# Kernel optimization log

Measured on AMD Instinct MI355X. Metric: run time of the kernel, lower is better.

Reference implementation:

```python
import jax, jax.numpy as jnp
import numpy as np

N = 100000
E = 50000
NNZ = 300000
F_IN = 128
F_OUT = 128


def setup_inputs() -> dict:
    key = jax.random.key(0)
    ks = jax.random.split(key, 10)
    X = jax.random.normal(ks[0], (N, F_IN), dtype=jnp.float32)
    X0 = jax.random.normal(ks[1], (N, F_IN), dtype=jnp.float32)
    vertex = jax.random.randint(ks[2], (NNZ,), 0, N, dtype=jnp.int32)
    edges = jax.random.randint(ks[3], (NNZ,), 0, E, dtype=jnp.int32)
    # params init per reset_parameters: uniform(0.02, 0.05)
    u = lambda k, s: jax.random.uniform(k, s, jnp.float32, 0.02, 0.05)
    w_b = u(ks[4], (2 * F_IN, F_OUT))
    w_a = u(ks[5], (2 * F_IN, F_OUT))
    w_c = u(ks[6], (2 * F_IN, F_OUT))
    b_b = u(ks[7], (1, F_OUT))
    b_a = u(ks[8], (1, F_OUT))
    b_c = u(ks[9], (1, F_OUT))
    return {"X": X, "vertex": vertex, "edges": edges, "X0": X0,
            "n_edges": E, "w_b": w_b, "w_a": w_a, "w_c": w_c,
            "b_b": b_b, "b_a": b_a, "b_c": b_c}


def reference(X, vertex, edges, X0, n_edges, w_b, w_a, w_c, b_b, b_a, b_c):
    n = X.shape[-2]
    # round 1: node -> hyperedge aggregation (scatter-add by edge id)
    Xve = X[vertex]                                        # [nnz, F]
    Xe = jax.ops.segment_sum(Xve, edges, num_segments=n_edges)  # [E, F]
    # round 2: hyperedge -> node, concat with gathered node features
    Xev = jnp.concatenate([X[vertex], Xe[edges]], axis=-1)  # [nnz, 2F]
    Xv = jax.ops.segment_sum(Xev, vertex, num_segments=n)   # [N, 2F]
    # normalization is Identity (InputNorm=False)
    center = Xv @ w_b + b_b                 # [N, F_OUT]
    aXv = jnp.abs(Xv)
    scope_l = aXv @ w_a + b_a
    scope_r = aXv @ w_c + b_c
    HL = center - scope_l
    HR = center + scope_r
    return (center, HL, HR)
```

## Files before the change

kernel.cpp:

```cpp
#include <hip/hip_runtime.h>
#include <cstddef>
#include <cstdint>

#define F 128
#define E_FIXED 50000
#define SCAN_ELEMS 2048

typedef __attribute__((ext_vector_type(8))) short short8;
typedef __attribute__((ext_vector_type(4))) float f32x4;
typedef __attribute__((ext_vector_type(4))) unsigned int uint32x4;
typedef __attribute__((address_space(3))) unsigned int lds_uint;
typedef const __attribute__((address_space(1))) unsigned int glb_uint;

__device__ inline unsigned short f32_to_bf16(float f) {
  union { float f; unsigned int u; } v; v.f = f;
  unsigned int u = v.u;
  unsigned int r = u + 0x7FFFu + ((u >> 16) & 1u);
  return (unsigned short)(r >> 16);
}

__global__ __launch_bounds__(256) void zero_kernel(int* __restrict__ p, int n4) {
  int i = blockIdx.x * 256 + threadIdx.x;
  if (i < n4) reinterpret_cast<int4*>(p)[i] = make_int4(0, 0, 0, 0);
}

__global__ __launch_bounds__(256) void count_kernel(
    const int* __restrict__ vertex, const int* __restrict__ edges,
    int* __restrict__ cnt, int nnz, int E) {
  int i = blockIdx.x * 256 + threadIdx.x;
  if (i >= nnz) return;
  atomicAdd(cnt + edges[i], 1);
  atomicAdd(cnt + E + vertex[i], 1);
}

__global__ __launch_bounds__(256) void scan_partial_kernel(
    const int* __restrict__ cnt, int* __restrict__ off,
    int* __restrict__ bsum, int L) {
  __shared__ int s[256];
  const int t = threadIdx.x;
  const int base = blockIdx.x * SCAN_ELEMS + t * 8;
  int v[8];
  if (base + 8 <= L) {
    int4 a = *reinterpret_cast<const int4*>(cnt + base);
    int4 b = *reinterpret_cast<const int4*>(cnt + base + 4);
    v[0] = a.x; v[1] = a.y; v[2] = a.z; v[3] = a.w;
    v[4] = b.x; v[5] = b.y; v[6] = b.z; v[7] = b.w;
  } else {
    #pragma unroll
    for (int j = 0; j < 8; ++j) v[j] = (base + j < L) ? cnt[base + j] : 0;
  }
  int tsum = 0;
  #pragma unroll
  for (int j = 0; j < 8; ++j) tsum += v[j];
  s[t] = tsum;
  __syncthreads();
  #pragma unroll
  for (int d = 1; d < 256; d <<= 1) {
    int val = (t >= d) ? s[t - d] : 0;
    __syncthreads();
    s[t] += val;
    __syncthreads();
  }
  int run = s[t] - tsum;
  #pragma unroll
  for (int j = 0; j < 8; ++j) {
    int idx = base + j;
    if (idx < L) off[idx] = run;
    run += v[j];
  }
  if (t == 255) bsum[blockIdx.x] = s[255];
}

__global__ __launch_bounds__(128) void scan_bsum_kernel(
    int* __restrict__ bsum, int nb) {
  __shared__ int s[128];
  int t = threadIdx.x;
  int val = (t < nb) ? bsum[t] : 0;
  s[t] = val;
  __syncthreads();
  #pragma unroll
  for (int d = 1; d < 128; d <<= 1) {
    int x = (t >= d) ? s[t - d] : 0;
    __syncthreads();
    s[t] += x;
    __syncthreads();
  }
  if (t < nb) bsum[t] = s[t] - val;
}

__global__ __launch_bounds__(256) void scan_add_kernel(
    int* __restrict__ off, const int* __restrict__ bsum, int L) {
  int b = blockIdx.x;
  if (b == 0) return;
  int add = bsum[b];
  int base = b * SCAN_ELEMS + threadIdx.x * 8;
  if (base + 8 <= L) {
    int4* p0 = reinterpret_cast<int4*>(off + base);
    int4* p1 = reinterpret_cast<int4*>(off + base + 4);
    int4 a = *p0, c = *p1;
    a.x += add; a.y += add; a.z += add; a.w += add;
    c.x += add; c.y += add; c.z += add; c.w += add;
    *p0 = a; *p1 = c;
  } else {
    #pragma unroll
    for (int j = 0; j < 8; ++j)
      if (base + j < L) off[base + j] += add;
  }
}

__global__ __launch_bounds__(256) void fill_kernel(
    const int* __restrict__ vertex, const int* __restrict__ edges,
    const int* __restrict__ off, int* __restrict__ cur,
    int* __restrict__ csr, int nnz, int E) {
  int i = blockIdx.x * 256 + threadIdx.x;
  if (i >= nnz) return;
  int v = vertex[i], e = edges[i];
  int p = atomicAdd(cur + e, 1);
  csr[off[e] + p] = v;
  int q = atomicAdd(cur + E + v, 1);
  csr[off[E + v] + q] = e;
}

__global__ __launch_bounds__(256) void gather_edge_kernel(
    const float* __restrict__ X, const int* __restrict__ off,
    const int* __restrict__ cnt, const int* __restrict__ csr,
    float* __restrict__ Xe, int E) {
  int gid = blockIdx.x * 256 + threadIdx.x;
  int e = gid >> 6;
  int lane = threadIdx.x & 63;
  if (e >= E) return;
  int start = off[e], n = cnt[e];
  float2 acc = make_float2(0.f, 0.f);
  for (int j = 0; j < n; ++j) {
    int v = csr[start + j];
    float2 x = *reinterpret_cast<const float2*>(X + (size_t)v * F + lane * 2);
    acc.x += x.x; acc.y += x.y;
  }
  *reinterpret_cast<float2*>(Xe + (size_t)e * F + lane * 2) = acc;
}

__global__ __launch_bounds__(256) void gather_vertex_kernel(
    const float* __restrict__ Xe, const int* __restrict__ off,
    const int* __restrict__ cnt, const int* __restrict__ csr,
    float* __restrict__ Xv2, int E, int N) {
  int gid = blockIdx.x * 256 + threadIdx.x;
  int v = gid >> 6;
  int lane = threadIdx.x & 63;
  if (v >= N) return;
  int start = off[E + v], n = cnt[E + v];
  float2 acc = make_float2(0.f, 0.f);
  for (int j = 0; j < n; ++j) {
    int e = csr[start + j];
    float2 x = *reinterpret_cast<const float2*>(Xe + (size_t)e * F + lane * 2);
    acc.x += x.x; acc.y += x.y;
  }
  *reinterpret_cast<float2*>(Xv2 + (size_t)v * F + lane * 2) = acc;
}

__global__ __launch_bounds__(256) void convert_w_kernel(
    const float* __restrict__ wb, const float* __restrict__ wa,
    const float* __restrict__ wc, unsigned short* __restrict__ wt) {
  int id = blockIdx.x * 256 + threadIdx.x;
  int mat = id >> 15;
  int r = id & 32767;
  int k = r >> 7;
  int col = r & 127;
  int ks = k >> 5;
  int kg = (k >> 3) & 3;
  int e  = k & 7;
  int ct = col >> 4;
  int bc = col & 15;
  int lane = kg * 16 + bc;
  const float* w = (mat == 0) ? wb : ((mat == 1) ? wa : wc);
  size_t off = ((((size_t)(ks * 3 + mat) * 8 + ct) * 64 + lane) * 8 + e);
  wt[off] = f32_to_bf16(w[r]);
}

__global__ __launch_bounds__(512, 4) void fused_mfma_kernel(
    const float* __restrict__ X, const float* __restrict__ Xv2,
    const int* __restrict__ deg,
    const unsigned short* __restrict__ wt,
    const float* __restrict__ bb, const float* __restrict__ ba,
    const float* __restrict__ bc,
    float* __restrict__ out, int N) {
  __shared__ unsigned short wlds[48 * 512];
  const int t = threadIdx.x;
  const int wave = t >> 6;
  const int lane = t & 63;
  const int node0 = blockIdx.x * 128;
  const int node = node0 + wave * 16 + (lane & 15);
  const int kg = lane >> 4;

  uint32x4 a[8];
  const bool ok = node < N;
  const float dg = ok ? (float)deg[node] : 0.f;
  #pragma unroll
  for (int ks = 0; ks < 8; ++ks) {
    float4 f0 = make_float4(0.f, 0.f, 0.f, 0.f);
    float4 f1 = make_float4(0.f, 0.f, 0.f, 0.f);
    if (ok) {
      const float* src = (ks < 4)
          ? X   + (size_t)node * F + ks * 32 + kg * 8
          : Xv2 + (size_t)node * F + (ks - 4) * 32 + kg * 8;
      f0 = *reinterpret_cast<const float4*>(src);
      f1 = *reinterpret_cast<const float4*>(src + 4);
      if (ks < 4) {
        f0.x *= dg; f0.y *= dg; f0.z *= dg; f0.w *= dg;
        f1.x *= dg; f1.y *= dg; f1.z *= dg; f1.w *= dg;
      }
    }
    uint32x4 p;
    p[0] = (unsigned int)f32_to_bf16(f0.x) | ((unsigned int)f32_to_bf16(f0.y) << 16);
    p[1] = (unsigned int)f32_to_bf16(f0.z) | ((unsigned int)f32_to_bf16(f0.w) << 16);
    p[2] = (unsigned int)f32_to_bf16(f1.x) | ((unsigned int)f32_to_bf16(f1.y) << 16);
    p[3] = (unsigned int)f32_to_bf16(f1.z) | ((unsigned int)f32_to_bf16(f1.w) << 16);
    a[ks] = p;
  }

  const int nrow0 = node0 + wave * 16 + (lane >> 4) * 4;

  #pragma unroll
  for (int h = 0; h < 4; ++h) {
    #pragma unroll
    for (int i = 0; i < 3; ++i) {
      int p = wave * 3 + i;
      #pragma unroll
      for (int c = 0; c < 2; ++c) {
        int g = p * 8 + h * 2 + c;
        int q = p * 2 + c;
        __builtin_amdgcn_global_load_lds(
            (glb_uint*)(wt + (size_t)g * 512 + lane * 8),
            (lds_uint*)(&wlds[q * 512]), 16, 0, 0);
      }
    }
    __syncthreads();

    f32x4 acc[3][2];
    #pragma unroll
    for (int m = 0; m < 3; ++m)
      #pragma unroll
      for (int c = 0; c < 2; ++c) acc[m][c] = (f32x4)(0.f);

    #pragma unroll
    for (int ks = 0; ks < 8; ++ks) {
      uint32x4 av = a[ks];
      uint32x4 aav = av & 0x7FFF7FFFu;
      short8 A  = __builtin_bit_cast(short8, av);
      short8 AA = __builtin_bit_cast(short8, aav);
      #pragma unroll
      for (int m = 0; m < 3; ++m) {
        short8 Ause = (m == 0) ? A : AA;
        #pragma unroll
        for (int c = 0; c < 2; ++c) {
          int q = (ks * 3 + m) * 2 + c;
          short8 B = *reinterpret_cast<const short8*>(&wlds[q * 512 + lane * 8]);
          acc[m][c] = __builtin_amdgcn_mfma_f32_16x16x32_bf16(Ause, B, acc[m][c], 0, 0, 0);
        }
      }
    }

    #pragma unroll
    for (int c = 0; c < 2; ++c) {
      int col = h * 32 + c * 16 + (lane & 15);
      float vb = bb[col], va = ba[col], vc = bc[col];
      #pragma unroll
      for (int j = 0; j < 4; ++j) {
        int nd = nrow0 + j;
        if (nd < N) {
          float ce = acc[0][c][j] + vb;
          float sl = acc[1][c][j] + va;
          float sr = acc[2][c][j] + vc;
          out[(size_t)nd * F + col] = ce;
          out[((size_t)N + nd) * F + col] = ce - sl;
          out[((size_t)2 * N + nd) * F + col] = ce + sr;
        }
      }
    }
    __syncthreads();
  }
}

extern "C" void kernel_launch(void* const* d_in, const int* in_sizes, int n_in,
                              void* d_out, int out_size, void* d_ws, size_t ws_size,
                              hipStream_t stream) {
  const float* X      = (const float*)d_in[0];
  const int*   vertex = (const int*)d_in[1];
  const int*   edges  = (const int*)d_in[2];
  const float* wb = (const float*)d_in[5];
  const float* wa = (const float*)d_in[6];
  const float* wc = (const float*)d_in[7];
  const float* bb = (const float*)d_in[8];
  const float* ba = (const float*)d_in[9];
  const float* bc = (const float*)d_in[10];

  const int N   = in_sizes[0] / F;
  const int nnz = in_sizes[1];
  const int E   = E_FIXED;
  const int L   = E + N;
  const int nb  = (L + SCAN_ELEMS - 1) / SCAN_ELEMS;

  float* Xe  = (float*)d_ws;
  float* Xv2 = Xe + (size_t)E * F;
  unsigned short* wt = (unsigned short*)(Xv2 + (size_t)N * F);
  int* cnt  = (int*)(wt + 3 * 32768);
  int* cur  = cnt + L;
  int* off  = cur + L;
  int* bsum = off + L;
  int* csr  = bsum + 128;

  int n4 = (2 * L) / 4;
  zero_kernel<<<(n4 + 255) / 256, 256, 0, stream>>>(cnt, n4);

  convert_w_kernel<<<384, 256, 0, stream>>>(wb, wa, wc, wt);

  int blocks_nnz = (nnz + 255) / 256;
  count_kernel<<<blocks_nnz, 256, 0, stream>>>(vertex, edges, cnt, nnz, E);

  scan_partial_kernel<<<nb, 256, 0, stream>>>(cnt, off, bsum, L);
  scan_bsum_kernel<<<1, 128, 0, stream>>>(bsum, nb);
  scan_add_kernel<<<nb, 256, 0, stream>>>(off, bsum, L);

  fill_kernel<<<blocks_nnz, 256, 0, stream>>>(vertex, edges, off, cur, csr, nnz, E);

  gather_edge_kernel<<<(E * 64 + 255) / 256, 256, 0, stream>>>(
      X, off, cnt, csr, Xe, E);
  gather_vertex_kernel<<<(N * 64 + 255) / 256, 256, 0, stream>>>(
      Xe, off, cnt, csr, Xv2, E, N);

  int blocks_g = (N + 127) / 128;
  fused_mfma_kernel<<<blocks_g, 512, 0, stream>>>(X, Xv2, cnt + E, wt,
                                                  bb, ba, bc, (float*)d_out, N);
}
```

Measured before the change: 224.8 us.

## Fuse vertex gather into MFMA kernel and store edge aggregates as bf16

Removes the separate gather_vertex kernel and the fp32 Xv2 intermediate. The edge-to-vertex sum is now computed inside the fused MFMA kernel and staged through LDS, and the edge aggregates Xe are written as bf16, which halves their footprint. This cuts one launch and a full N×F fp32 write/read round trip. In exchange the edge sums are rounded to bf16 before the second aggregation, adding precision loss. Each wave also runs a serial per-row gather loop before the matmul, which may reduce latency hiding.

```diff
diff --git a/kernel.cpp b/kernel.cpp
--- a/kernel.cpp
+++ b/kernel.cpp
@@ -124,7 +124,7 @@
 __global__ __launch_bounds__(256) void gather_edge_kernel(
     const float* __restrict__ X, const int* __restrict__ off,
     const int* __restrict__ cnt, const int* __restrict__ csr,
-    float* __restrict__ Xe, int E) {
+    unsigned short* __restrict__ Xe_b, int E) {
   int gid = blockIdx.x * 256 + threadIdx.x;
   int e = gid >> 6;
   int lane = threadIdx.x & 63;
@@ -136,25 +136,9 @@
     float2 x = *reinterpret_cast<const float2*>(X + (size_t)v * F + lane * 2);
     acc.x += x.x; acc.y += x.y;
   }
-  *reinterpret_cast<float2*>(Xe + (size_t)e * F + lane * 2) = acc;
-}
-
-__global__ __launch_bounds__(256) void gather_vertex_kernel(
-    const float* __restrict__ Xe, const int* __restrict__ off,
-    const int* __restrict__ cnt, const int* __restrict__ csr,
-    float* __restrict__ Xv2, int E, int N) {
-  int gid = blockIdx.x * 256 + threadIdx.x;
-  int v = gid >> 6;
-  int lane = threadIdx.x & 63;
-  if (v >= N) return;
-  int start = off[E + v], n = cnt[E + v];
-  float2 acc = make_float2(0.f, 0.f);
-  for (int j = 0; j < n; ++j) {
-    int e = csr[start + j];
-    float2 x = *reinterpret_cast<const float2*>(Xe + (size_t)e * F + lane * 2);
-    acc.x += x.x; acc.y += x.y;
-  }
-  *reinterpret_cast<float2*>(Xv2 + (size_t)v * F + lane * 2) = acc;
+  unsigned int pk = (unsigned int)f32_to_bf16(acc.x) |
+                    ((unsigned int)f32_to_bf16(acc.y) << 16);
+  *reinterpret_cast<unsigned int*>(Xe_b + (size_t)e * F + lane * 2) = pk;
 }
 
 __global__ __launch_bounds__(256) void convert_w_kernel(
@@ -177,13 +161,16 @@
 }
 
 __global__ __launch_bounds__(512, 4) void fused_mfma_kernel(
-    const float* __restrict__ X, const float* __restrict__ Xv2,
-    const int* __restrict__ deg,
+    const float* __restrict__ X,
+    const unsigned short* __restrict__ Xe_b,
+    const int* __restrict__ offv,
+    const int* __restrict__ cntv,
+    const int* __restrict__ csr,
     const unsigned short* __restrict__ wt,
     const float* __restrict__ bb, const float* __restrict__ ba,
     const float* __restrict__ bc,
     float* __restrict__ out, int N) {
-  __shared__ unsigned short wlds[48 * 512];
+  __shared__ unsigned short lds_buf[48 * 512];
   const int t = threadIdx.x;
   const int wave = t >> 6;
   const int lane = t & 63;
@@ -191,23 +178,40 @@
   const int node = node0 + wave * 16 + (lane & 15);
   const int kg = lane >> 4;
 
+  unsigned short* tile = lds_buf;
+  #pragma unroll 1
+  for (int i = 0; i < 16; ++i) {
+    int nd = node0 + wave * 16 + i;
+    float2 acc = make_float2(0.f, 0.f);
+    if (nd < N) {
+      int start = offv[nd], n = cntv[nd];
+      for (int j = 0; j < n; ++j) {
+        int e = csr[start + j];
+        unsigned int u = *reinterpret_cast<const unsigned int*>(
+            Xe_b + (size_t)e * F + lane * 2);
+        union { unsigned int u; float f; } lo, hi;
+        lo.u = u << 16; hi.u = u & 0xFFFF0000u;
+        acc.x += lo.f; acc.y += hi.f;
+      }
+    }
+    unsigned int pk = (unsigned int)f32_to_bf16(acc.x) |
+                      ((unsigned int)f32_to_bf16(acc.y) << 16);
+    *reinterpret_cast<unsigned int*>(tile + (wave * 16 + i) * 136 + lane * 2) = pk;
+  }
+
   uint32x4 a[8];
   const bool ok = node < N;
-  const float dg = ok ? (float)deg[node] : 0.f;
-  #pragma unroll
-  for (int ks = 0; ks < 8; ++ks) {
+  const float dg = ok ? (float)cntv[node] : 0.f;
+  #pragma unroll
+  for (int ks = 0; ks < 4; ++ks) {
     float4 f0 = make_float4(0.f, 0.f, 0.f, 0.f);
     float4 f1 = make_float4(0.f, 0.f, 0.f, 0.f);
     if (ok) {
-      const float* src = (ks < 4)
-          ? X   + (size_t)node * F + ks * 32 + kg * 8
-          : Xv2 + (size_t)node * F + (ks - 4) * 32 + kg * 8;
+      const float* src = X + (size_t)node * F + ks * 32 + kg * 8;
       f0 = *reinterpret_cast<const float4*>(src);
       f1 = *reinterpret_cast<const float4*>(src + 4);
-      if (ks < 4) {
-        f0.x *= dg; f0.y *= dg; f0.z *= dg; f0.w *= dg;
-        f1.x *= dg; f1.y *= dg; f1.z *= dg; f1.w *= dg;
-      }
+      f0.x *= dg; f0.y *= dg; f0.z *= dg; f0.w *= dg;
+      f1.x *= dg; f1.y *= dg; f1.z *= dg; f1.w *= dg;
     }
     uint32x4 p;
     p[0] = (unsigned int)f32_to_bf16(f0.x) | ((unsigned int)f32_to_bf16(f0.y) << 16);
@@ -216,6 +220,15 @@
     p[3] = (unsigned int)f32_to_bf16(f1.z) | ((unsigned int)f32_to_bf16(f1.w) << 16);
     a[ks] = p;
   }
+  {
+    const int arow = wave * 16 + (lane & 15);
+    #pragma unroll
+    for (int ks = 4; ks < 8; ++ks) {
+      const unsigned short* p = tile + arow * 136 + (ks - 4) * 32 + kg * 8;
+      a[ks] = *reinterpret_cast<const uint32x4*>(p);
+    }
+  }
+  __syncthreads();
 
   const int nrow0 = node0 + wave * 16 + (lane >> 4) * 4;
 
@@ -230,7 +243,7 @@
         int q = p * 2 + c;
         __builtin_amdgcn_global_load_lds(
             (glb_uint*)(wt + (size_t)g * 512 + lane * 8),
-            (lds_uint*)(&wlds[q * 512]), 16, 0, 0);
+            (lds_uint*)(&lds_buf[q * 512]), 16, 0, 0);
       }
     }
     __syncthreads();
@@ -253,7 +266,7 @@
         #pragma unroll
         for (int c = 0; c < 2; ++c) {
           int q = (ks * 3 + m) * 2 + c;
-          short8 B = *reinterpret_cast<const short8*>(&wlds[q * 512 + lane * 8]);
+          short8 B = *reinterpret_cast<const short8*>(&lds_buf[q * 512 + lane * 8]);
           acc[m][c] = __builtin_amdgcn_mfma_f32_16x16x32_bf16(Ause, B, acc[m][c], 0, 0, 0);
         }
       }
@@ -299,9 +312,8 @@
   const int L   = E + N;
   const int nb  = (L + SCAN_ELEMS - 1) / SCAN_ELEMS;
 
-  float* Xe  = (float*)d_ws;
-  float* Xv2 = Xe + (size_t)E * F;
-  unsigned short* wt = (unsigned short*)(Xv2 + (size_t)N * F);
+  unsigned short* Xe_b = (unsigned short*)d_ws;
+  unsigned short* wt = Xe_b + (size_t)E * F;
   int* cnt  = (int*)(wt + 3 * 32768);
   int* cur  = cnt + L;
   int* off  = cur + L;
@@ -323,11 +335,9 @@
   fill_kernel<<<blocks_nnz, 256, 0, stream>>>(vertex, edges, off, cur, csr, nnz, E);
 
   gather_edge_kernel<<<(E * 64 + 255) / 256, 256, 0, stream>>>(
-      X, off, cnt, csr, Xe, E);
-  gather_vertex_kernel<<<(N * 64 + 255) / 256, 256, 0, stream>>>(
-      Xe, off, cnt, csr, Xv2, E, N);
+      X, off, cnt, csr, Xe_b, E);
 
   int blocks_g = (N + 127) / 128;
-  fused_mfma_kernel<<<blocks_g, 512, 0, stream>>>(X, Xv2, cnt + E, wt,
-                                                  bb, ba, bc, (float*)d_out, N);
-}
+  fused_mfma_kernel<<<blocks_g, 512, 0, stream>>>(
+      X, Xe_b, off + E, cnt + E, csr, wt, bb, ba, bc, (float*)d_out, N);
+}
```

Result: slower. 234.9 us (+4.5%).
